# Performance work log

Measured on AMD Instinct MI355X. Metric: run time of the kernel, lower is better.

Reference implementation:

```python
import jax, jax.numpy as jnp
import numpy as np

H = 16  # head_num

def _rope(x, cos, sin):
    # x: [B,H,T,dh]; cos/sin: [T, dh//2]
    xr = x.reshape(*x.shape[:-1], -1, 2)
    re, im = xr[..., 0], xr[..., 1]
    out_re = re * cos - im * sin
    out_im = re * sin + im * cos
    return jnp.stack([out_re, out_im], axis=-1).reshape(x.shape)

def setup_inputs() -> dict:
    key = jax.random.key(0)
    ks = jax.random.split(key, 5)
    B, T, D = 2, 2048, 1024
    s = 1.0 / np.sqrt(D)
    return {
        "embedding_word": jax.random.normal(ks[0], (B, T, D), jnp.float32),
        "wq": jax.random.normal(ks[1], (D, D), jnp.float32) * s,
        "wk": jax.random.normal(ks[2], (D, D), jnp.float32) * s,
        "wv": jax.random.normal(ks[3], (D, D), jnp.float32) * s,
        "wo": jax.random.normal(ks[4], (D, D), jnp.float32) * s,
    }

def reference(embedding_word, wq, wk, wv, wo):
    x = embedding_word
    B, T, D = x.shape
    dh = D // H
    # projections (torch Linear: x @ W.T)
    q = (x @ wq.T).reshape(B, T, H, dh).transpose(0, 2, 1, 3)  # [B,H,T,dh]
    k = (x @ wk.T).reshape(B, T, H, dh).transpose(0, 2, 1, 3)
    v = (x @ wv.T).reshape(B, T, H, dh).transpose(0, 2, 1, 3)
    # rotary embedding (theta=10000)
    freqs = 1.0 / (10000.0 ** (jnp.arange(0, dh, 2, dtype=jnp.float32) / dh))
    ang = jnp.arange(T, dtype=jnp.float32)[:, None] * freqs[None, :]  # [T, dh/2]
    cos, sin = jnp.cos(ang), jnp.sin(ang)
    q = _rope(q, cos, sin)
    k = _rope(k, cos, sin)
    # attention with causal mask; scale after mask as in original
    scores = jnp.einsum("bhqd,bhkd->bhqk", q, k)
    causal = jnp.triu(jnp.ones((T, T), dtype=bool), k=1)
    scores = jnp.where(causal, -jnp.inf, scores)
    weights = jax.nn.softmax(scores / jnp.sqrt(jnp.float32(dh)), axis=-1)
    out = jnp.einsum("bhqk,bhkd->bhqd", weights, v)
    out = out.transpose(0, 2, 1, 3).reshape(B, T, D)
    return out @ wo.T
```

## Files before the change

### kernel.cpp

```cpp
#include <hip/hip_runtime.h>
#include <hip/hip_bf16.h>
#include <math.h>

#define B_  2
#define T_  2048
#define D_  1024
#define H_  16
#define TOK (B_*T_)

typedef __attribute__((ext_vector_type(8)))  short bf16x8;
typedef __attribute__((ext_vector_type(4)))  float f32x4;
typedef __attribute__((ext_vector_type(16))) float f32x16;

static __device__ __forceinline__ float bf2f(short u) {
    union { unsigned int i; float f; } c;
    c.i = ((unsigned int)(unsigned short)u) << 16;
    return c.f;
}
static __device__ __forceinline__ short f2bf(float f) {
    union { float f; unsigned int i; } c; c.f = f;
    unsigned int r = c.i + 0x7fff + ((c.i >> 16) & 1);
    return (short)(r >> 16);
}
static __device__ __forceinline__ unsigned cvtpk(float lo, float hi2) {
    unsigned r;
    asm("v_cvt_pk_bf16_f32 %0, %1, %2" : "=v"(r) : "v"(lo), "v"(hi2));
    return r;
}

__global__ __launch_bounds__(256) void cast_table(
    const float* __restrict__ x,  const float* __restrict__ wq,
    const float* __restrict__ wk, const float* __restrict__ wv,
    const float* __restrict__ wo,
    short* __restrict__ xb,  short* __restrict__ wqb,
    short* __restrict__ wkb, short* __restrict__ wvb,
    short* __restrict__ wob, float2* __restrict__ tab)
{
    const int bid = blockIdx.x;
    if (bid >= 4096) {
        int idx = (bid - 4096) * 256 + threadIdx.x;
        int t = idx >> 5, i = idx & 31;
        float freq = __powf(10000.f, -(float)i * (1.0f / 32.0f));
        float s, c;
        sincosf((float)t * freq, &s, &c);
        tab[idx] = make_float2(c, s);
        return;
    }
    int i = bid * 256 + threadIdx.x;
    const float* src; short* dst; int off;
    if (i < 524288) { src = x; dst = xb; off = i; }
    else {
        int j = i - 524288;
        int wsel = j >> 17;  off = j & 131071;
        src = wsel == 0 ? wq : wsel == 1 ? wk : wsel == 2 ? wv : wo;
        dst = wsel == 0 ? wqb : wsel == 1 ? wkb : wsel == 2 ? wvb : wob;
    }
    const float4* p = reinterpret_cast<const float4*>(src);
    float4 a = p[2*off], b = p[2*off+1];
    bf16x8 o;
    o[0] = f2bf(a.x); o[1] = f2bf(a.y); o[2] = f2bf(a.z); o[3] = f2bf(a.w);
    o[4] = f2bf(b.x); o[5] = f2bf(b.y); o[6] = f2bf(b.z); o[7] = f2bf(b.w);
    reinterpret_cast<bf16x8*>(dst)[off] = o;
}

__global__ __launch_bounds__(256) void rope_apply2(short* __restrict__ Q,
                                                   short* __restrict__ K,
                                                   const float2* __restrict__ tab)
{
    int g = blockIdx.x * 256 + threadIdx.x;
    short* X;
    float sc;
    int q;
    if (g < 524288) { X = Q; sc = 0.18033688011112042f; q = g; }
    else            { X = K; sc = 1.0f;                 q = g - 524288; }
    int p0 = q << 2;
    int tt = (p0 >> 9) & (T_ - 1);
    int i0 = p0 & 31;
    int4 v = reinterpret_cast<int4*>(X)[q];
    int out[4]; int vv[4] = {v.x, v.y, v.z, v.w};
#pragma unroll
    for (int j = 0; j < 4; ++j) {
        float2 cs = tab[tt * 32 + i0 + j];
        float re = bf2f((short)(vv[j] & 0xffff));
        float im = bf2f((short)(((unsigned int)vv[j]) >> 16));
        float nr = (re * cs.x - im * cs.y) * sc;
        float ni = (re * cs.y + im * cs.x) * sc;
        out[j] = (int)(unsigned short)f2bf(nr) |
                 ((int)(unsigned short)f2bf(ni) << 16);
    }
    reinterpret_cast<int4*>(X)[q] = make_int4(out[0], out[1], out[2], out[3]);
}

template<int BF16OUT>
__global__ __launch_bounds__(256) void gemm_abt_mfma(
    const short* __restrict__ A,
    const short* __restrict__ B0, const short* __restrict__ B1, const short* __restrict__ B2,
    short* __restrict__ Ob0, short* __restrict__ Ob1, short* __restrict__ Ob2,
    float* __restrict__ Of0, int K)
{
    __shared__ short As[128 * 32];
    __shared__ short Bs[128 * 32];
    __shared__ short Tb[128 * 136];
    const int sel = blockIdx.x >> 3;
    const int bn  = (blockIdx.x & 7) << 7;
    const int bm  = blockIdx.y << 7;
    const short* Bm = sel == 0 ? B0 : (sel == 1 ? B1 : B2);
    short* Obp      = sel == 0 ? Ob0 : (sel == 1 ? Ob1 : Ob2);
    const int tid  = threadIdx.x;
    const int wv   = tid >> 6, lane = tid & 63;
    const int wr   = wv >> 1,  wc   = wv & 1;
    const int fr   = lane & 15, fg  = lane >> 4;
    const int srow  = lane >> 2;
    const int skoff = (lane & 3) << 3;
    f32x4 acc[4][4] = {};

    for (int k0 = 0; k0 < K; k0 += 32) {
        __syncthreads();
#pragma unroll
        for (int it = 0; it < 2; ++it) {
            const int c = wv * 2 + it;
            const int r = 16 * c + srow;
            __builtin_amdgcn_global_load_lds(
                (const __attribute__((address_space(1))) unsigned int*)
                    (A + (size_t)(bm + r) * K + k0 + skoff),
                (__attribute__((address_space(3))) unsigned int*)(As + c * 512),
                16, 0, 0);
            __builtin_amdgcn_global_load_lds(
                (const __attribute__((address_space(1))) unsigned int*)
                    (Bm + (size_t)(bn + r) * K + k0 + skoff),
                (__attribute__((address_space(3))) unsigned int*)(Bs + c * 512),
                16, 0, 0);
        }
        __syncthreads();
        bf16x8 af[4], bfr[4];
#pragma unroll
        for (int m = 0; m < 4; ++m)
            af[m] = *(const bf16x8*)(As + (wr * 64 + m * 16 + fr) * 32 + fg * 8);
#pragma unroll
        for (int n = 0; n < 4; ++n)
            bfr[n] = *(const bf16x8*)(Bs + (wc * 64 + n * 16 + fr) * 32 + fg * 8);
#pragma unroll
        for (int m = 0; m < 4; ++m)
#pragma unroll
            for (int n = 0; n < 4; ++n)
                acc[m][n] = __builtin_amdgcn_mfma_f32_16x16x32_bf16(
                                af[m], bfr[n], acc[m][n], 0, 0, 0);
    }

    if (BF16OUT && sel == 2) {
#pragma unroll
        for (int m = 0; m < 4; ++m)
#pragma unroll
            for (int n = 0; n < 4; ++n) {
                const int dl = wc * 64 + n * 16 + fr;
                const int tk = wr * 64 + m * 16 + fg * 4;
                unsigned lo  = cvtpk(acc[m][n][0], acc[m][n][1]);
                unsigned hi2 = cvtpk(acc[m][n][2], acc[m][n][3]);
                *(unsigned*)(Tb + dl * 136 + tk)     = lo;
                *(unsigned*)(Tb + dl * 136 + tk + 2) = hi2;
            }
        __syncthreads();
        const int bb = bm >> 11;
#pragma unroll
        for (int it = 0; it < 8; ++it) {
            const int c  = it * 256 + tid;
            const int dl = c >> 4;
            const int off = (c & 15) << 3;
            bf16x8 v = *(const bf16x8*)(Tb + dl * 136 + off);
            *(bf16x8*)(Obp + (size_t)(bb * 1024 + bn + dl) * 2048
                             + (bm & 2047) + off) = v;
        }
        return;
    }

    const int row0 = bm + wr * 64 + fg * 4;
    const int col0 = bn + wc * 64 + fr;
#pragma unroll
    for (int m = 0; m < 4; ++m)
#pragma unroll
        for (int n = 0; n < 4; ++n)
#pragma unroll
            for (int j = 0; j < 4; ++j) {
                const size_t idx = (size_t)(row0 + m * 16 + j) * 1024 + col0 + n * 16;
                if (BF16OUT) Obp[idx] = f2bf(acc[m][n][j]);
                else         Of0[idx] = acc[m][n][j];
            }
}

__global__ __launch_bounds__(256) void attn_v3(
    const short* __restrict__ Qb, const short* __restrict__ Kb,
    const short* __restrict__ Vt, short* __restrict__ Ob)
{
    __shared__ unsigned Ot[4 * 1152];

    const int tid = threadIdx.x;
    const int w = tid >> 6, lane = tid & 63;
    const int ql = lane & 31, hi = lane >> 5;
    const int dd = (int)blockIdx.x;
    const int L  = (dd & 7) * 64 + (dd >> 3);
    const int bh = L >> 4;
    const int qb = 15 - (L & 15);
    const int b  = bh >> 4, h = bh & 15;
    const int q0 = qb * 128 + w * 32;
    const int q_glob = q0 + ql;
    const int nt = (q0 >> 6) + 1;

    const short* qp = Qb + (size_t)(b * T_ + q_glob) * D_ + h * 64 + hi * 8;
    bf16x8 qf[4];
#pragma unroll
    for (int ds = 0; ds < 4; ++ds)
        qf[ds] = *(const bf16x8*)(qp + 16 * ds);

    float m_run = -3e38f, l_run = 0.f;
    f32x16 accO0, accO1;
#pragma unroll
    for (int r = 0; r < 16; ++r) { accO0[r] = 0.f; accO1[r] = 0.f; }

    const short* kbase = Kb + (size_t)(b * T_) * D_ + h * 64 + hi * 8;
    const short* vbase = Vt + (size_t)(bh * 64) * 2048 + hi * 8;

    for (int t = 0; t < nt; ++t) {
        const int K0 = t << 6;
        const bool diag  = (K0 + 63 > q0);
        const bool useHi = (K0 + 32 <= q0 + 31);

        const short* kp = kbase + (size_t)K0 * D_;
        bf16x8 kf0[4], kf1[4];
#pragma unroll
        for (int ds = 0; ds < 4; ++ds)
            kf0[ds] = *(const bf16x8*)(kp + (size_t)ql * D_ + 16 * ds);
        if (useHi) {
#pragma unroll
            for (int ds = 0; ds < 4; ++ds)
                kf1[ds] = *(const bf16x8*)(kp + (size_t)(32 + ql) * D_ + 16 * ds);
        }

        f32x16 s0, s1;
#pragma unroll
        for (int r = 0; r < 16; ++r) { s0[r] = 0.f; s1[r] = 0.f; }
#pragma unroll
        for (int ds = 0; ds < 4; ++ds)
            s0 = __builtin_amdgcn_mfma_f32_32x32x16_bf16(kf0[ds], qf[ds], s0, 0, 0, 0);
        if (useHi) {
#pragma unroll
            for (int ds = 0; ds < 4; ++ds)
                s1 = __builtin_amdgcn_mfma_f32_32x32x16_bf16(kf1[ds], qf[ds], s1, 0, 0, 0);
        }

        if (diag) {
            const int qrel = q_glob - K0;
#pragma unroll
            for (int r = 0; r < 16; ++r) {
                const int kv0 = 4 * hi + (r & 3) + 8 * (r >> 2);
                s0[r] = (kv0 <= qrel) ? s0[r] : -3e38f;
            }
            if (useHi) {
#pragma unroll
                for (int r = 0; r < 16; ++r) {
                    const int kv0 = 4 * hi + (r & 3) + 8 * (r >> 2);
                    s1[r] = (kv0 + 32 <= qrel) ? s1[r] : -3e38f;
                }
            }
        }

        float mloc = s0[0];
#pragma unroll
        for (int r = 1; r < 16; ++r) mloc = fmaxf(mloc, s0[r]);
        if (useHi) {
#pragma unroll
            for (int r = 0; r < 16; ++r) mloc = fmaxf(mloc, s1[r]);
        }
        mloc = fmaxf(mloc, __shfl_xor(mloc, 32));
        if (!__all(mloc <= m_run + 11.5f)) {
            const float mnew = fmaxf(m_run, mloc);
            const float corr = exp2f(m_run - mnew);
            m_run = mnew;
            l_run *= corr;
#pragma unroll
            for (int r = 0; r < 16; ++r) { accO0[r] *= corr; accO1[r] *= corr; }
        }
        float lsum = 0.f;
#pragma unroll
        for (int r = 0; r < 16; ++r) { s0[r] = exp2f(s0[r] - m_run); lsum += s0[r]; }
        if (useHi) {
#pragma unroll
            for (int r = 0; r < 16; ++r) { s1[r] = exp2f(s1[r] - m_run); lsum += s1[r]; }
        }
        lsum += __shfl_xor(lsum, 32);
        l_run += lsum;

        unsigned W[8][2];
#pragma unroll
        for (int q4 = 0; q4 < 4; ++q4) {
            W[q4][0] = cvtpk(s0[4*q4+0], s0[4*q4+1]);
            W[q4][1] = cvtpk(s0[4*q4+2], s0[4*q4+3]);
        }
        if (useHi) {
#pragma unroll
            for (int q4 = 0; q4 < 4; ++q4) {
                W[q4 + 4][0] = cvtpk(s1[4*q4+0], s1[4*q4+1]);
                W[q4 + 4][1] = cvtpk(s1[4*q4+2], s1[4*q4+3]);
            }
        }

#pragma unroll
        for (int sl = 0; sl < 4; ++sl) {
            if (sl < 2 || useHi) {
                const int qe = 2 * sl, qo = qe + 1;
                unsigned srcA = hi ? W[qe][0] : W[qo][0];
                unsigned srcB = hi ? W[qe][1] : W[qo][1];
                unsigned xA = (unsigned)__shfl_xor((int)srcA, 32);
                unsigned xB = (unsigned)__shfl_xor((int)srcB, 32);
                union { unsigned u[4]; bf16x8 v; } pu;
                pu.u[0] = hi ? xA : W[qe][0];
                pu.u[1] = hi ? xB : W[qe][1];
                pu.u[2] = hi ? W[qo][0] : xA;
                pu.u[3] = hi ? W[qo][1] : xB;
                bf16x8 vf0 = *(const bf16x8*)(vbase + (size_t)ql * 2048        + K0 + 16 * sl);
                bf16x8 vf1 = *(const bf16x8*)(vbase + (size_t)(32 + ql) * 2048 + K0 + 16 * sl);
                accO0 = __builtin_amdgcn_mfma_f32_32x32x16_bf16(vf0, pu.v, accO0, 0, 0, 0);
                accO1 = __builtin_amdgcn_mfma_f32_32x32x16_bf16(vf1, pu.v, accO1, 0, 0, 0);
            }
        }
    }

    const float invl = 1.f / l_run;
#pragma unroll
    for (int rq = 0; rq < 4; ++rq) {
        unsigned p0 = cvtpk(accO0[4*rq+0] * invl, accO0[4*rq+1] * invl);
        unsigned p1 = cvtpk(accO0[4*rq+2] * invl, accO0[4*rq+3] * invl);
        unsigned p2 = cvtpk(accO1[4*rq+0] * invl, accO1[4*rq+1] * invl);
        unsigned p3 = cvtpk(accO1[4*rq+2] * invl, accO1[4*rq+3] * invl);
        const int du0 = 4 * rq + 2 * hi;
        Ot[w * 1152 + ql * 36 + du0]      = p0;
        Ot[w * 1152 + ql * 36 + du0 + 1]  = p1;
        Ot[w * 1152 + ql * 36 + du0 + 16] = p2;
        Ot[w * 1152 + ql * 36 + du0 + 17] = p3;
    }
    __syncthreads();
    {
        const int qq = tid >> 1, half = tid & 1;
        const int4* s4 = (const int4*)(Ot + (qq >> 5) * 1152 + (qq & 31) * 36 + half * 16);
        int4* d4 = (int4*)(Ob + (size_t)(b * T_ + qb * 128 + qq) * D_ + h * 64 + half * 32);
        d4[0] = s4[0]; d4[1] = s4[1]; d4[2] = s4[2]; d4[3] = s4[3];
    }
}

extern "C" void kernel_launch(void* const* d_in, const int* in_sizes, int n_in,
                              void* d_out, int out_size, void* d_ws, size_t ws_size,
                              hipStream_t stream)
{
    const float* x  = (const float*)d_in[0];
    const float* wq = (const float*)d_in[1];
    const float* wk = (const float*)d_in[2];
    const float* wv = (const float*)d_in[3];
    const float* wo = (const float*)d_in[4];
    float* out = (float*)d_out;

    const size_t NTOK = (size_t)TOK * D_;
    const size_t NW   = (size_t)D_ * D_;
    short* xb  = (short*)d_ws;
    short* wqb = xb  + NTOK;
    short* wkb = wqb + NW;
    short* wvb = wkb + NW;
    short* wob = wvb + NW;
    short* Qb  = wob + NW;
    short* Kb  = Qb  + NTOK;
    short* Vtr = Kb  + NTOK;
    short* Obf = Vtr + NTOK;
    float2* tab = (float2*)(Obf + NTOK);

    cast_table<<<4352, 256, 0, stream>>>(x, wq, wk, wv, wo,
                                         xb, wqb, wkb, wvb, wob, tab);

    gemm_abt_mfma<1><<<dim3(24, 32), 256, 0, stream>>>(
        xb, wqb, wkb, wvb, Qb, Kb, Vtr, nullptr, D_);

    rope_apply2<<<4096, 256, 0, stream>>>(Qb, Kb, tab);

    attn_v3<<<512, 256, 0, stream>>>(Qb, Kb, Vtr, Obf);

    gemm_abt_mfma<0><<<dim3(8, 32), 256, 0, stream>>>(
        Obf, wob, wob, wob, nullptr, nullptr, nullptr, out, D_);
}
```

Measured before the change: 280.1 us.

## Pair complementary causal query tiles per wave sharing K/V loads with double-buffered K

Rewrites the attention kernel so each wave processes two 32-row query tiles at opposite ends of the causal triangle (rank p and 63-p). Every wave then does a balanced amount of work, and each K/V tile load serves both query tiles. K tiles are double-buffered via register prefetch of the next tile, and cross-half reductions use permlane32_swap with tree-style max/sum. Blocks shrink to 128 threads with launch_bounds(128,1). This raises register pressure considerably and lowers occupancy, which may hurt latency hiding.

```diff
diff --git a/kernel.cpp b/kernel.cpp
--- a/kernel.cpp
+++ b/kernel.cpp
@@ -26,6 +26,14 @@
     unsigned r;
     asm("v_cvt_pk_bf16_f32 %0, %1, %2" : "=v"(r) : "v"(lo), "v"(hi2));
     return r;
+}
+static __device__ __forceinline__ float xhalf_max(float x) {
+    auto pr = __builtin_amdgcn_permlane32_swap(__float_as_int(x), __float_as_int(x), false, false);
+    return fmaxf(__int_as_float(pr[0]), __int_as_float(pr[1]));
+}
+static __device__ __forceinline__ float xhalf_add(float x) {
+    auto pr = __builtin_amdgcn_permlane32_swap(__float_as_int(x), __float_as_int(x), false, false);
+    return __int_as_float(pr[0]) + __int_as_float(pr[1]);
 }
 
 __global__ __launch_bounds__(256) void cast_table(
@@ -187,162 +195,243 @@
             }
 }
 
-__global__ __launch_bounds__(256) void attn_v3(
+struct KBuf { bf16x8 k0[4], k1[4]; };
+
+static __device__ __forceinline__ void load_k(KBuf& kb, const short* kbase,
+                                              int ql, int t, int qmaxB)
+{
+    const int K0 = t << 6;
+    const bool hiN = (K0 + 32 <= qmaxB);
+    const short* kp  = kbase + (size_t)(K0 + ql) * D_;
+#pragma unroll
+    for (int ds = 0; ds < 4; ++ds)
+        kb.k0[ds] = *(const bf16x8*)(kp + 16 * ds);
+    if (hiN) {
+        const short* kph = kp + (size_t)32 * D_;
+#pragma unroll
+        for (int ds = 0; ds < 4; ++ds)
+            kb.k1[ds] = *(const bf16x8*)(kph + 16 * ds);
+    }
+}
+
+static __device__ __forceinline__ void load_v(bf16x8* v0, bf16x8* v1,
+                                              const short* vbase, int ql,
+                                              int K0, bool hiB)
+{
+    const short* vp0 = vbase + (size_t)ql * 2048 + K0;
+    const short* vp1 = vbase + (size_t)(32 + ql) * 2048 + K0;
+#pragma unroll
+    for (int sl = 0; sl < 4; ++sl) if (sl < 2 || hiB) {
+        v0[sl] = *(const bf16x8*)(vp0 + 16 * sl);
+        v1[sl] = *(const bf16x8*)(vp1 + 16 * sl);
+    }
+}
+
+static __device__ __forceinline__ void qk_phase(const KBuf& kb, const bf16x8* qf,
+                                                f32x16& s0, f32x16& s1, bool useHi)
+{
+#pragma unroll
+    for (int r = 0; r < 16; ++r) { s0[r] = 0.f; s1[r] = 0.f; }
+#pragma unroll
+    for (int ds = 0; ds < 4; ++ds)
+        s0 = __builtin_amdgcn_mfma_f32_32x32x16_bf16(kb.k0[ds], qf[ds], s0, 0, 0, 0);
+    if (useHi) {
+#pragma unroll
+        for (int ds = 0; ds < 4; ++ds)
+            s1 = __builtin_amdgcn_mfma_f32_32x32x16_bf16(kb.k1[ds], qf[ds], s1, 0, 0, 0);
+    }
+}
+
+static __device__ __forceinline__ void stream_tail(
+    f32x16& s0, f32x16& s1, f32x16& a0, f32x16& a1,
+    float& m_run, float& l_run,
+    const bf16x8* v0, const bf16x8* v1,
+    int qg, int K0, bool diag, bool useHi, int hi)
+{
+    if (diag) {
+        const int qrel = qg - K0;
+#pragma unroll
+        for (int r = 0; r < 16; ++r) {
+            const int kv0 = 4*hi + (r & 3) + 8*(r >> 2);
+            s0[r] = (kv0 <= qrel) ? s0[r] : -3e38f;
+        }
+        if (useHi) {
+#pragma unroll
+            for (int r = 0; r < 16; ++r) {
+                const int kv0 = 4*hi + (r & 3) + 8*(r >> 2);
+                s1[r] = (kv0 + 32 <= qrel) ? s1[r] : -3e38f;
+            }
+        }
+    }
+    float mt[8];
+#pragma unroll
+    for (int r = 0; r < 8; ++r) mt[r] = fmaxf(s0[2*r], s0[2*r+1]);
+    if (useHi) {
+#pragma unroll
+        for (int r = 0; r < 8; ++r) mt[r] = fmaxf(mt[r], fmaxf(s1[2*r], s1[2*r+1]));
+    }
+#pragma unroll
+    for (int r = 0; r < 4; ++r) mt[r] = fmaxf(mt[r], mt[r+4]);
+    float mloc = fmaxf(fmaxf(mt[0], mt[1]), fmaxf(mt[2], mt[3]));
+    mloc = xhalf_max(mloc);
+    if (!__all(mloc <= m_run + 11.5f)) {
+        const float mnew = fmaxf(m_run, mloc);
+        const float corr = exp2f(m_run - mnew);
+        m_run = mnew; l_run *= corr;
+#pragma unroll
+        for (int r = 0; r < 16; ++r) { a0[r] *= corr; a1[r] *= corr; }
+    }
+#pragma unroll
+    for (int r = 0; r < 16; ++r) s0[r] = exp2f(s0[r] - m_run);
+    if (useHi) {
+#pragma unroll
+        for (int r = 0; r < 16; ++r) s1[r] = exp2f(s1[r] - m_run);
+    }
+    float lt[8];
+#pragma unroll
+    for (int r = 0; r < 8; ++r) lt[r] = s0[2*r] + s0[2*r+1];
+    if (useHi) {
+#pragma unroll
+        for (int r = 0; r < 8; ++r) lt[r] += s1[2*r] + s1[2*r+1];
+    }
+#pragma unroll
+    for (int r = 0; r < 4; ++r) lt[r] += lt[r+4];
+    l_run += xhalf_add((lt[0] + lt[1]) + (lt[2] + lt[3]));
+
+    unsigned W[8][2];
+#pragma unroll
+    for (int q4 = 0; q4 < 4; ++q4) {
+        W[q4][0] = cvtpk(s0[4*q4+0], s0[4*q4+1]);
+        W[q4][1] = cvtpk(s0[4*q4+2], s0[4*q4+3]);
+    }
+    if (useHi) {
+#pragma unroll
+        for (int q4 = 0; q4 < 4; ++q4) {
+            W[q4+4][0] = cvtpk(s1[4*q4+0], s1[4*q4+1]);
+            W[q4+4][1] = cvtpk(s1[4*q4+2], s1[4*q4+3]);
+        }
+    }
+#pragma unroll
+    for (int sl = 0; sl < 4; ++sl) if (sl < 2 || useHi) {
+        const int qe = 2*sl, qo = qe + 1;
+        unsigned srcA = hi ? W[qe][0] : W[qo][0];
+        unsigned srcB = hi ? W[qe][1] : W[qo][1];
+        unsigned xA = (unsigned)__shfl_xor((int)srcA, 32);
+        unsigned xB = (unsigned)__shfl_xor((int)srcB, 32);
+        union { unsigned u[4]; bf16x8 v; } pu;
+        pu.u[0] = hi ? xA : W[qe][0];
+        pu.u[1] = hi ? xB : W[qe][1];
+        pu.u[2] = hi ? W[qo][0] : xA;
+        pu.u[3] = hi ? W[qo][1] : xB;
+        a0 = __builtin_amdgcn_mfma_f32_32x32x16_bf16(v0[sl], pu.v, a0, 0, 0, 0);
+        a1 = __builtin_amdgcn_mfma_f32_32x32x16_bf16(v1[sl], pu.v, a1, 0, 0, 0);
+    }
+}
+
+static __device__ __forceinline__ void epi_stream(unsigned* Ot, int region, int ql,
+    int hi, const f32x16& a0, const f32x16& a1, float l_run)
+{
+    const float invl = 1.f / l_run;
+#pragma unroll
+    for (int rq = 0; rq < 4; ++rq) {
+        unsigned p0 = cvtpk(a0[4*rq+0]*invl, a0[4*rq+1]*invl);
+        unsigned p1 = cvtpk(a0[4*rq+2]*invl, a0[4*rq+3]*invl);
+        unsigned p2 = cvtpk(a1[4*rq+0]*invl, a1[4*rq+1]*invl);
+        unsigned p3 = cvtpk(a1[4*rq+2]*invl, a1[4*rq+3]*invl);
+        const int du0 = 4*rq + 2*hi;
+        Ot[region*1152 + ql*36 + du0]      = p0;
+        Ot[region*1152 + ql*36 + du0 + 1]  = p1;
+        Ot[region*1152 + ql*36 + du0 + 16] = p2;
+        Ot[region*1152 + ql*36 + du0 + 17] = p3;
+    }
+}
+
+#define COMPUTE_TILE(KB, tt) do {                                             \
+    const int K0 = (tt) << 6;                                                 \
+    const bool actA = ((tt) < ntA);                                           \
+    const bool hiB = (K0 + 32 <= qmaxB), dgB = (K0 + 63 > q0B);               \
+    bf16x8 v0[4], v1[4];                                                      \
+    load_v(v0, v1, vbase, ql, K0, hiB);                                       \
+    f32x16 sA0, sA1, sB0, sB1;                                                \
+    if (actA) {                                                               \
+        const bool hiA = (K0 + 32 <= qmaxA);                                  \
+        qk_phase(KB, qfA, sA0, sA1, hiA);                                     \
+    }                                                                         \
+    qk_phase(KB, qfB, sB0, sB1, hiB);                                         \
+    if (actA) {                                                               \
+        const bool hiA = (K0 + 32 <= qmaxA), dgA = (K0 + 63 > q0A);           \
+        stream_tail(sA0, sA1, aA0, aA1, mA, lA, v0, v1, qgA, K0, dgA, hiA, hi); \
+    }                                                                         \
+    stream_tail(sB0, sB1, aB0, aB1, mB, lB, v0, v1, qgB, K0, dgB, hiB, hi);   \
+} while (0)
+
+__global__ __launch_bounds__(128, 1) void attn_v4(
     const short* __restrict__ Qb, const short* __restrict__ Kb,
     const short* __restrict__ Vt, short* __restrict__ Ob)
 {
     __shared__ unsigned Ot[4 * 1152];
-
     const int tid = threadIdx.x;
     const int w = tid >> 6, lane = tid & 63;
     const int ql = lane & 31, hi = lane >> 5;
-    const int dd = (int)blockIdx.x;
-    const int L  = (dd & 7) * 64 + (dd >> 3);
-    const int bh = L >> 4;
-    const int qb = 15 - (L & 15);
-    const int b  = bh >> 4, h = bh & 15;
-    const int q0 = qb * 128 + w * 32;
-    const int q_glob = q0 + ql;
-    const int nt = (q0 >> 6) + 1;
-
-    const short* qp = Qb + (size_t)(b * T_ + q_glob) * D_ + h * 64 + hi * 8;
-    bf16x8 qf[4];
-#pragma unroll
-    for (int ds = 0; ds < 4; ++ds)
-        qf[ds] = *(const bf16x8*)(qp + 16 * ds);
-
-    float m_run = -3e38f, l_run = 0.f;
-    f32x16 accO0, accO1;
-#pragma unroll
-    for (int r = 0; r < 16; ++r) { accO0[r] = 0.f; accO1[r] = 0.f; }
+    const int g = (int)blockIdx.x;
+    const int xcd = g & 7, j = g >> 3;
+    const int bh = xcd * 4 + (j >> 4);
+    const int pb = j & 15;
+    const int p  = pb * 2 + w;
+    const int rankA = p, rankB = 63 - p;
+    const int b = bh >> 4, h = bh & 15;
+
+    const int q0A = rankA * 32, q0B = rankB * 32;
+    const int qgA = q0A + ql,   qgB = q0B + ql;
+    const int qmaxA = q0A + 31, qmaxB = q0B + 31;
+    const int ntA = (rankA >> 1) + 1, ntB = (rankB >> 1) + 1;
+
+    bf16x8 qfA[4], qfB[4];
+    {
+        const short* qpA = Qb + (size_t)(b * T_ + qgA) * D_ + h * 64 + hi * 8;
+        const short* qpB = Qb + (size_t)(b * T_ + qgB) * D_ + h * 64 + hi * 8;
+#pragma unroll
+        for (int ds = 0; ds < 4; ++ds) {
+            qfA[ds] = *(const bf16x8*)(qpA + 16 * ds);
+            qfB[ds] = *(const bf16x8*)(qpB + 16 * ds);
+        }
+    }
+
+    float mA = -3e38f, lA = 0.f, mB = -3e38f, lB = 0.f;
+    f32x16 aA0, aA1, aB0, aB1;
+#pragma unroll
+    for (int r = 0; r < 16; ++r) { aA0[r]=0.f; aA1[r]=0.f; aB0[r]=0.f; aB1[r]=0.f; }
 
     const short* kbase = Kb + (size_t)(b * T_) * D_ + h * 64 + hi * 8;
     const short* vbase = Vt + (size_t)(bh * 64) * 2048 + hi * 8;
 
-    for (int t = 0; t < nt; ++t) {
-        const int K0 = t << 6;
-        const bool diag  = (K0 + 63 > q0);
-        const bool useHi = (K0 + 32 <= q0 + 31);
-
-        const short* kp = kbase + (size_t)K0 * D_;
-        bf16x8 kf0[4], kf1[4];
-#pragma unroll
-        for (int ds = 0; ds < 4; ++ds)
-            kf0[ds] = *(const bf16x8*)(kp + (size_t)ql * D_ + 16 * ds);
-        if (useHi) {
-#pragma unroll
-            for (int ds = 0; ds < 4; ++ds)
-                kf1[ds] = *(const bf16x8*)(kp + (size_t)(32 + ql) * D_ + 16 * ds);
-        }
-
-        f32x16 s0, s1;
-#pragma unroll
-        for (int r = 0; r < 16; ++r) { s0[r] = 0.f; s1[r] = 0.f; }
-#pragma unroll
-        for (int ds = 0; ds < 4; ++ds)
-            s0 = __builtin_amdgcn_mfma_f32_32x32x16_bf16(kf0[ds], qf[ds], s0, 0, 0, 0);
-        if (useHi) {
-#pragma unroll
-            for (int ds = 0; ds < 4; ++ds)
-                s1 = __builtin_amdgcn_mfma_f32_32x32x16_bf16(kf1[ds], qf[ds], s1, 0, 0, 0);
-        }
-
-        if (diag) {
-            const int qrel = q_glob - K0;
-#pragma unroll
-            for (int r = 0; r < 16; ++r) {
-                const int kv0 = 4 * hi + (r & 3) + 8 * (r >> 2);
-                s0[r] = (kv0 <= qrel) ? s0[r] : -3e38f;
-            }
-            if (useHi) {
-#pragma unroll
-                for (int r = 0; r < 16; ++r) {
-                    const int kv0 = 4 * hi + (r & 3) + 8 * (r >> 2);
-                    s1[r] = (kv0 + 32 <= qrel) ? s1[r] : -3e38f;
-                }
-            }
-        }
-
-        float mloc = s0[0];
-#pragma unroll
-        for (int r = 1; r < 16; ++r) mloc = fmaxf(mloc, s0[r]);
-        if (useHi) {
-#pragma unroll
-            for (int r = 0; r < 16; ++r) mloc = fmaxf(mloc, s1[r]);
-        }
-        mloc = fmaxf(mloc, __shfl_xor(mloc, 32));
-        if (!__all(mloc <= m_run + 11.5f)) {
-            const float mnew = fmaxf(m_run, mloc);
-            const float corr = exp2f(m_run - mnew);
-            m_run = mnew;
-            l_run *= corr;
-#pragma unroll
-            for (int r = 0; r < 16; ++r) { accO0[r] *= corr; accO1[r] *= corr; }
-        }
-        float lsum = 0.f;
-#pragma unroll
-        for (int r = 0; r < 16; ++r) { s0[r] = exp2f(s0[r] - m_run); lsum += s0[r]; }
-        if (useHi) {
-#pragma unroll
-            for (int r = 0; r < 16; ++r) { s1[r] = exp2f(s1[r] - m_run); lsum += s1[r]; }
-        }
-        lsum += __shfl_xor(lsum, 32);
-        l_run += lsum;
-
-        unsigned W[8][2];
-#pragma unroll
-        for (int q4 = 0; q4 < 4; ++q4) {
-            W[q4][0] = cvtpk(s0[4*q4+0], s0[4*q4+1]);
-            W[q4][1] = cvtpk(s0[4*q4+2], s0[4*q4+3]);
-        }
-        if (useHi) {
-#pragma unroll
-            for (int q4 = 0; q4 < 4; ++q4) {
-                W[q4 + 4][0] = cvtpk(s1[4*q4+0], s1[4*q4+1]);
-                W[q4 + 4][1] = cvtpk(s1[4*q4+2], s1[4*q4+3]);
-            }
-        }
-
-#pragma unroll
-        for (int sl = 0; sl < 4; ++sl) {
-            if (sl < 2 || useHi) {
-                const int qe = 2 * sl, qo = qe + 1;
-                unsigned srcA = hi ? W[qe][0] : W[qo][0];
-                unsigned srcB = hi ? W[qe][1] : W[qo][1];
-                unsigned xA = (unsigned)__shfl_xor((int)srcA, 32);
-                unsigned xB = (unsigned)__shfl_xor((int)srcB, 32);
-                union { unsigned u[4]; bf16x8 v; } pu;
-                pu.u[0] = hi ? xA : W[qe][0];
-                pu.u[1] = hi ? xB : W[qe][1];
-                pu.u[2] = hi ? W[qo][0] : xA;
-                pu.u[3] = hi ? W[qo][1] : xB;
-                bf16x8 vf0 = *(const bf16x8*)(vbase + (size_t)ql * 2048        + K0 + 16 * sl);
-                bf16x8 vf1 = *(const bf16x8*)(vbase + (size_t)(32 + ql) * 2048 + K0 + 16 * sl);
-                accO0 = __builtin_amdgcn_mfma_f32_32x32x16_bf16(vf0, pu.v, accO0, 0, 0, 0);
-                accO1 = __builtin_amdgcn_mfma_f32_32x32x16_bf16(vf1, pu.v, accO1, 0, 0, 0);
-            }
-        }
-    }
-
-    const float invl = 1.f / l_run;
-#pragma unroll
-    for (int rq = 0; rq < 4; ++rq) {
-        unsigned p0 = cvtpk(accO0[4*rq+0] * invl, accO0[4*rq+1] * invl);
-        unsigned p1 = cvtpk(accO0[4*rq+2] * invl, accO0[4*rq+3] * invl);
-        unsigned p2 = cvtpk(accO1[4*rq+0] * invl, accO1[4*rq+1] * invl);
-        unsigned p3 = cvtpk(accO1[4*rq+2] * invl, accO1[4*rq+3] * invl);
-        const int du0 = 4 * rq + 2 * hi;
-        Ot[w * 1152 + ql * 36 + du0]      = p0;
-        Ot[w * 1152 + ql * 36 + du0 + 1]  = p1;
-        Ot[w * 1152 + ql * 36 + du0 + 16] = p2;
-        Ot[w * 1152 + ql * 36 + du0 + 17] = p3;
-    }
+    KBuf bufA, bufB;
+    load_k(bufA, kbase, ql, 0, qmaxB);
+    int t = 0; bool cA = true;
+    while (true) {
+        if (t + 1 < ntB) {
+            if (cA) load_k(bufB, kbase, ql, t + 1, qmaxB);
+            else    load_k(bufA, kbase, ql, t + 1, qmaxB);
+        }
+        if (cA) COMPUTE_TILE(bufA, t); else COMPUTE_TILE(bufB, t);
+        ++t;
+        if (t >= ntB) break;
+        cA = !cA;
+    }
+
+    epi_stream(Ot, w * 2 + 0, ql, hi, aA0, aA1, lA);
+    epi_stream(Ot, w * 2 + 1, ql, hi, aB0, aB1, lB);
     __syncthreads();
     {
-        const int qq = tid >> 1, half = tid & 1;
-        const int4* s4 = (const int4*)(Ot + (qq >> 5) * 1152 + (qq & 31) * 36 + half * 16);
-        int4* d4 = (int4*)(Ob + (size_t)(b * T_ + qb * 128 + qq) * D_ + h * 64 + half * 32);
-        d4[0] = s4[0]; d4[1] = s4[1]; d4[2] = s4[2]; d4[3] = s4[3];
+        const int r = tid >> 5, row = tid & 31;
+        const int w_ = r >> 1, s_ = r & 1;
+        const int p_ = pb * 2 + w_;
+        const int rank = s_ ? (63 - p_) : p_;
+        const unsigned* src = Ot + r * 1152 + row * 36;
+        short* drow = Ob + (size_t)(b * T_ + rank * 32 + row) * D_ + h * 64;
+#pragma unroll
+        for (int e = 0; e < 8; ++e)
+            ((int4*)drow)[e] = ((const int4*)src)[e];
     }
 }
 
@@ -378,7 +467,7 @@
 
     rope_apply2<<<4096, 256, 0, stream>>>(Qb, Kb, tab);
 
-    attn_v3<<<512, 256, 0, stream>>>(Qb, Kb, Vtr, Obf);
+    attn_v4<<<512, 128, 0, stream>>>(Qb, Kb, Vtr, Obf);
 
     gemm_abt_mfma<0><<<dim3(8, 32), 256, 0, stream>>>(
         Obf, wob, wob, wob, nullptr, nullptr, nullptr, out, D_);
```

New measurement: 340.6 us. +21.6%, slower.

## Split attention into single-wave blocks with longest-first scheduling

Applied to the files above, without the earlier changes.

The attention kernel now runs one wavefront (64 threads) per block instead of four, with 2048 blocks each covering 32 query rows of one batch-head. Blocks are ordered so the longest causal rows go first, and launch bounds request several blocks per SIMD. The aim is better load balance across CUs for the triangular causal workload and removal of the 4-wave block tail imbalance. The cost is more blocks to launch and no K/V sharing between waves through a common block.

```diff
diff --git a/kernel.cpp b/kernel.cpp
--- a/kernel.cpp
+++ b/kernel.cpp
@@ -187,23 +187,21 @@
             }
 }
 
-__global__ __launch_bounds__(256) void attn_v3(
+__global__ __launch_bounds__(64, 4) void attn_v5(
     const short* __restrict__ Qb, const short* __restrict__ Kb,
     const short* __restrict__ Vt, short* __restrict__ Ob)
 {
-    __shared__ unsigned Ot[4 * 1152];
-
-    const int tid = threadIdx.x;
-    const int w = tid >> 6, lane = tid & 63;
+    __shared__ unsigned Ot[1152];
+
+    const int lane = threadIdx.x;
     const int ql = lane & 31, hi = lane >> 5;
-    const int dd = (int)blockIdx.x;
-    const int L  = (dd & 7) * 64 + (dd >> 3);
-    const int bh = L >> 4;
-    const int qb = 15 - (L & 15);
-    const int b  = bh >> 4, h = bh & 15;
-    const int q0 = qb * 128 + w * 32;
+    const int bid = (int)blockIdx.x;
+    const int rank = 63 - (bid >> 5);
+    const int bh  = bid & 31;
+    const int b   = bh >> 4, h = bh & 15;
+    const int q0  = rank * 32;
     const int q_glob = q0 + ql;
-    const int nt = (q0 >> 6) + 1;
+    const int nt  = (rank >> 1) + 1;
 
     const short* qp = Qb + (size_t)(b * T_ + q_glob) * D_ + h * 64 + hi * 8;
     bf16x8 qf[4];
@@ -332,16 +330,16 @@
         unsigned p2 = cvtpk(accO1[4*rq+0] * invl, accO1[4*rq+1] * invl);
         unsigned p3 = cvtpk(accO1[4*rq+2] * invl, accO1[4*rq+3] * invl);
         const int du0 = 4 * rq + 2 * hi;
-        Ot[w * 1152 + ql * 36 + du0]      = p0;
-        Ot[w * 1152 + ql * 36 + du0 + 1]  = p1;
-        Ot[w * 1152 + ql * 36 + du0 + 16] = p2;
-        Ot[w * 1152 + ql * 36 + du0 + 17] = p3;
+        Ot[ql * 36 + du0]      = p0;
+        Ot[ql * 36 + du0 + 1]  = p1;
+        Ot[ql * 36 + du0 + 16] = p2;
+        Ot[ql * 36 + du0 + 17] = p3;
     }
     __syncthreads();
     {
-        const int qq = tid >> 1, half = tid & 1;
-        const int4* s4 = (const int4*)(Ot + (qq >> 5) * 1152 + (qq & 31) * 36 + half * 16);
-        int4* d4 = (int4*)(Ob + (size_t)(b * T_ + qb * 128 + qq) * D_ + h * 64 + half * 32);
+        const int row = lane >> 1, half = lane & 1;
+        const int4* s4 = (const int4*)(Ot + row * 36 + half * 16);
+        int4* d4 = (int4*)(Ob + (size_t)(b * T_ + q0 + row) * D_ + h * 64 + half * 32);
         d4[0] = s4[0]; d4[1] = s4[1]; d4[2] = s4[2]; d4[3] = s4[3];
     }
 }
@@ -378,7 +376,7 @@
 
     rope_apply2<<<4096, 256, 0, stream>>>(Qb, Kb, tab);
 
-    attn_v3<<<512, 256, 0, stream>>>(Qb, Kb, Vtr, Obf);
+    attn_v5<<<2048, 64, 0, stream>>>(Qb, Kb, Vtr, Obf);
 
     gemm_abt_mfma<0><<<dim3(8, 32), 256, 0, stream>>>(
         Obf, wob, wob, wob, nullptr, nullptr, nullptr, out, D_);
```

Result: faster. 274.6 us (-2.0%).
